# Optimization experiments

Measured on AMD Instinct MI355X. Metric: run time of the kernel, lower is better.

The kernel has to match this reference:

```python
import jax, jax.numpy as jnp
import numpy as np

B, N, D = 4, 4096, 128


def setup_inputs() -> dict:
    key = jax.random.key(0)
    k1, k2, k3 = jax.random.split(key, 3)
    x = jax.random.normal(k1, (B, N, D), dtype=jnp.float32)
    # random 0/1 adjacency (float, matching torch usage where adj>0 is masked)
    adj_mat = jax.random.randint(k2, (B, N, N), 0, 2).astype(jnp.float32)
    # xavier_normal_ for square [D, D]: std = sqrt(2 / (D + D))
    U = jax.random.normal(k3, (D, D), dtype=jnp.float32) * np.sqrt(2.0 / (D + D))
    return {"x": x, "adj_mat": adj_mat, "U": U}


def reference(x, adj_mat, U):
    # per-node loop in the original is equivalent to a masked adj^T matmul:
    # new_x[b,i,:] = relu( (sum_j 1[adj[b,j,i] > 0] * x[b,j,:]) @ U / deg[b,i] )
    # with deg = adj.sum(axis=1), i.e. deg[b,i] = sum_j adj[b,j,i].
    mask = (adj_mat > 0).astype(x.dtype)            # [B, N, N]
    deg = jnp.sum(adj_mat, axis=1)                  # [B, N]
    agg = jnp.einsum("bji,bjd->bid", mask, x)       # [B, N, D]
    out = jax.nn.relu(jnp.einsum("bid,de->bie", agg, U) / deg[..., None])
    return out
```

## Files before the change

kernel.cpp:

```cpp
#include <hip/hip_runtime.h>
#include <hip/hip_bf16.h>
#include <stdint.h>

#define BB 4
#define NN 4096
#define DD 128
#define BI 64
#define BJ 64

typedef _Float16 f16;
typedef __attribute__((ext_vector_type(8))) _Float16 f16x8;
typedef __attribute__((ext_vector_type(4))) float f32x4;

typedef __attribute__((address_space(3))) uint32_t lds_u32_t;
typedef const __attribute__((address_space(1))) uint32_t glb_u32_t;

__device__ __forceinline__ void gload_lds16(const void* g, void* l) {
    __builtin_amdgcn_global_load_lds((glb_u32_t*)g, (lds_u32_t*)l, 16, 0, 0);
}

__global__ void prep_xt(const float* __restrict__ x, f16* __restrict__ xt) {
    __shared__ float tile[32][33];
    int bid = blockIdx.x;
    int b = bid >> 9;
    int rest = bid & 511;
    int j0 = (rest >> 2) * 32;
    int d0 = (rest & 3) * 32;
    int t = threadIdx.x;
#pragma unroll
    for (int p = 0; p < 4; ++p) {
        int idx = p * 256 + t;
        int jj = idx >> 5, dd = idx & 31;
        tile[jj][dd] = x[((size_t)b * NN + j0 + jj) * DD + d0 + dd];
    }
    __syncthreads();
#pragma unroll
    for (int p = 0; p < 4; ++p) {
        int idx = p * 256 + t;
        int dd = idx >> 5, jj = idx & 31;
        xt[((size_t)b * DD + d0 + dd) * NN + j0 + jj] = (f16)tile[jj][dd];
    }
}

__global__ void prep_ut(const float* __restrict__ U, f16* __restrict__ ut) {
    __shared__ float tile[32][33];
    int bid = blockIdx.x;
    int d0 = (bid >> 2) * 32, e0 = (bid & 3) * 32;
    int t = threadIdx.x;
#pragma unroll
    for (int p = 0; p < 4; ++p) {
        int idx = p * 256 + t;
        int dd = idx >> 5, ee = idx & 31;
        tile[dd][ee] = U[(size_t)(d0 + dd) * DD + e0 + ee];
    }
    __syncthreads();
#pragma unroll
    for (int p = 0; p < 4; ++p) {
        int idx = p * 256 + t;
        int ee = idx >> 5, dd = idx & 31;
        ut[(size_t)(e0 + ee) * DD + d0 + dd] = (f16)tile[dd][ee];
    }
}

__global__ __launch_bounds__(512, 2) void agg_kernel(
    const float* __restrict__ adj, const f16* __restrict__ xt,
    float* __restrict__ agg, float* __restrict__ deg)
{
    __shared__ __align__(16) f16 mlds[2][BI * BJ];
    __shared__ __align__(16) f16 xlds[2][DD * BJ];
    __shared__ float degl[8][BI];

    const int t = threadIdx.x;
    const int w = t >> 6;
    const int l = t & 63;
    const int bid = blockIdx.x;
    const int b = bid >> 6;
    const int i0 = (bid & 63) * BI;

    const float* adjb = adj + (size_t)b * NN * NN + i0;
    const f16* xtb = xt + (size_t)b * DD * NN;

    const int si = l;
    const int su = w;
    const int mwoff = (si * 8 + (su ^ ((si >> 1) & 7))) * 8;

    const int ifr = (w & 3) * 16;
    const int dbase = (w >> 2) * 64;

    f32x4 acc[4] = {f32x4{0,0,0,0}, f32x4{0,0,0,0}, f32x4{0,0,0,0}, f32x4{0,0,0,0}};
    float degp = 0.f;

    auto stage = [&](int jt, int buf) {
        const int j0 = jt * BJ;
#pragma unroll
        for (int c = 0; c < 2; ++c) {
            int g = (w * 2 + c) * 64 + l;
            int d = g >> 3, ul = g & 7;
            int ug = ul ^ ((d >> 1) & 7);
            gload_lds16(xtb + (size_t)d * NN + j0 + ug * 8, &xlds[buf][(size_t)g * 8]);
        }
        const float* src = adjb + (size_t)(j0 + su * 8) * NN + si;
        float v[8];
#pragma unroll
        for (int q = 0; q < 8; ++q) v[q] = src[(size_t)q * NN];
        f16x8 m8;
#pragma unroll
        for (int q = 0; q < 8; ++q) {
            degp += v[q];
            m8[q] = v[q] > 0.f ? (f16)1.f : (f16)0.f;
        }
        *(f16x8*)&mlds[buf][mwoff] = m8;
    };

    auto compute = [&](int buf) {
#pragma unroll
        for (int kk = 0; kk < 2; ++kk) {
            const int row = ifr + (l & 15);
            const int ug = kk * 4 + (l >> 4);
            f16x8 a = *(const f16x8*)&mlds[buf][(row * 8 + (ug ^ ((row >> 1) & 7))) * 8];
#pragma unroll
            for (int f = 0; f < 4; ++f) {
                const int d = dbase + f * 16 + (l & 15);
                f16x8 bb = *(const f16x8*)&xlds[buf][(d * 8 + (ug ^ ((d >> 1) & 7))) * 8];
                acc[f] = __builtin_amdgcn_mfma_f32_16x16x32_f16(a, bb, acc[f], 0, 0, 0);
            }
        }
    };

    stage(0, 0);
    for (int jt = 0; jt < NN / BJ; ++jt) {
        const int cur = jt & 1;
        __syncthreads();
        if (jt + 1 < NN / BJ) stage(jt + 1, cur ^ 1);
        compute(cur);
    }

    degl[w][l] = degp;
    __syncthreads();
    if (t < BI) {
        float s = 0.f;
#pragma unroll
        for (int q = 0; q < 8; ++q) s += degl[q][t];
        deg[b * NN + i0 + t] = s;
    }

    float* aggb = agg + ((size_t)b * NN + i0) * DD;
#pragma unroll
    for (int f = 0; f < 4; ++f) {
#pragma unroll
        for (int r = 0; r < 4; ++r) {
            int row = ifr + (l >> 4) * 4 + r;
            int col = dbase + f * 16 + (l & 15);
            aggb[(size_t)row * DD + col] = acc[f][r];
        }
    }
}

__global__ __launch_bounds__(256, 2) void out_kernel(
    const float* __restrict__ agg, const f16* __restrict__ ut,
    const float* __restrict__ deg, float* __restrict__ out)
{
    __shared__ __align__(16) f16 alds[64 * DD];
    __shared__ __align__(16) f16 ulds[DD * DD];

    const int t = threadIdx.x;
    const int w = t >> 6, l = t & 63;
    const int row0 = blockIdx.x * 64;

#pragma unroll
    for (int c = 0; c < 8; ++c) {
        int g = (w * 8 + c) * 64 + l;
        int e = g >> 4, ul = g & 15;
        int ug = ul ^ (e & 7);
        gload_lds16(ut + (size_t)e * DD + ug * 8, &ulds[(size_t)g * 8]);
    }
#pragma unroll
    for (int p = 0; p < 4; ++p) {
        int chunk = p * 256 + t;
        int row = chunk >> 4, ug = chunk & 15;
        const float* src = agg + (size_t)(row0 + row) * DD + ug * 8;
        f16x8 tmp;
#pragma unroll
        for (int q = 0; q < 8; ++q) tmp[q] = (f16)src[q];
        *(f16x8*)&alds[(row * 16 + (ug ^ (row & 7))) * 8] = tmp;
    }
    __syncthreads();

    f32x4 acc[8] = {f32x4{0,0,0,0}, f32x4{0,0,0,0}, f32x4{0,0,0,0}, f32x4{0,0,0,0},
                    f32x4{0,0,0,0}, f32x4{0,0,0,0}, f32x4{0,0,0,0}, f32x4{0,0,0,0}};
#pragma unroll
    for (int kk = 0; kk < 4; ++kk) {
        const int row = w * 16 + (l & 15);
        const int ug = kk * 4 + (l >> 4);
        f16x8 a = *(const f16x8*)&alds[(row * 16 + (ug ^ (row & 7))) * 8];
#pragma unroll
        for (int ef = 0; ef < 8; ++ef) {
            const int e = ef * 16 + (l & 15);
            f16x8 bb = *(const f16x8*)&ulds[(e * 16 + (ug ^ (e & 7))) * 8];
            acc[ef] = __builtin_amdgcn_mfma_f32_16x16x32_f16(a, bb, acc[ef], 0, 0, 0);
        }
    }

    float rdeg[4];
#pragma unroll
    for (int r = 0; r < 4; ++r)
        rdeg[r] = 1.0f / deg[row0 + w * 16 + (l >> 4) * 4 + r];

    float* outb = out + (size_t)(row0 + w * 16) * DD;
#pragma unroll
    for (int ef = 0; ef < 8; ++ef) {
#pragma unroll
        for (int r = 0; r < 4; ++r) {
            float vv = acc[ef][r] * rdeg[r];
            outb[(size_t)((l >> 4) * 4 + r) * DD + ef * 16 + (l & 15)] = vv > 0.f ? vv : 0.f;
        }
    }
}

extern "C" void kernel_launch(void* const* d_in, const int* in_sizes, int n_in,
                              void* d_out, int out_size, void* d_ws, size_t ws_size,
                              hipStream_t stream) {
    const float* x   = (const float*)d_in[0];
    const float* adj = (const float*)d_in[1];
    const float* U   = (const float*)d_in[2];
    float* out = (float*)d_out;

    char* ws = (char*)d_ws;
    f16* xt  = (f16*)ws;
    f16* ut  = (f16*)(ws + (size_t)BB * DD * NN * 2);
    float* agg = (float*)(ws + (size_t)BB * DD * NN * 2 + DD * DD * 2);
    float* deg = (float*)((char*)agg + (size_t)BB * NN * DD * 4);

    hipLaunchKernelGGL(prep_xt, dim3(BB * (NN / 32) * (DD / 32)), dim3(256), 0, stream, x, xt);
    hipLaunchKernelGGL(prep_ut, dim3((DD / 32) * (DD / 32)), dim3(256), 0, stream, U, ut);
    hipLaunchKernelGGL(agg_kernel, dim3(BB * (NN / BI)), dim3(512), 0, stream, adj, xt, agg, deg);
    hipLaunchKernelGGL(out_kernel, dim3((BB * NN) / 64), dim3(256), 0, stream, agg, ut, deg, out);
}
```

Measured before the change: 384.9 us.

## Fuse output GEMM into aggregation kernel and prefetch adj into registers before compute

The per-tile adjacency loads are now issued into registers before the MFMA compute on the current buffer, and converted to the f16 mask afterwards, so global load latency overlaps with compute. The separate output kernel is fused into the aggregation kernel's epilogue: the accumulator is written to LDS as f16, U is DMA'd into reused LDS, and the degree-scaled ReLU output is written directly. This removes the fp32 agg/deg round trip through global memory and one launch. The cost is higher register pressure from holding the prefetched values, plus a longer epilogue per block.

Result: no change. 383.0 us (-0.5%).

```diff
diff --git a/kernel.cpp b/kernel.cpp
--- a/kernel.cpp
+++ b/kernel.cpp
@@ -7,6 +7,7 @@
 #define DD 128
 #define BI 64
 #define BJ 64
+#define NT (NN / BJ)
 
 typedef _Float16 f16;
 typedef __attribute__((ext_vector_type(8))) _Float16 f16x8;
@@ -62,13 +63,14 @@
     }
 }
 
-__global__ __launch_bounds__(512, 2) void agg_kernel(
+__global__ __launch_bounds__(512, 2) void fused_kernel(
     const float* __restrict__ adj, const f16* __restrict__ xt,
-    float* __restrict__ agg, float* __restrict__ deg)
+    const f16* __restrict__ ut, float* __restrict__ out)
 {
     __shared__ __align__(16) f16 mlds[2][BI * BJ];
     __shared__ __align__(16) f16 xlds[2][DD * BJ];
     __shared__ float degl[8][BI];
+    __shared__ float degs[BI];
 
     const int t = threadIdx.x;
     const int w = t >> 6;
@@ -89,8 +91,14 @@
 
     f32x4 acc[4] = {f32x4{0,0,0,0}, f32x4{0,0,0,0}, f32x4{0,0,0,0}, f32x4{0,0,0,0}};
     float degp = 0.f;
-
-    auto stage = [&](int jt, int buf) {
+    float v[8];
+
+    auto load_adj = [&](int jt) {
+        const float* src = adjb + (size_t)(jt * BJ + su * 8) * NN + si;
+#pragma unroll
+        for (int q = 0; q < 8; ++q) v[q] = src[(size_t)q * NN];
+    };
+    auto dma_xt = [&](int jt, int buf) {
         const int j0 = jt * BJ;
 #pragma unroll
         for (int c = 0; c < 2; ++c) {
@@ -99,10 +107,8 @@
             int ug = ul ^ ((d >> 1) & 7);
             gload_lds16(xtb + (size_t)d * NN + j0 + ug * 8, &xlds[buf][(size_t)g * 8]);
         }
-        const float* src = adjb + (size_t)(j0 + su * 8) * NN + si;
-        float v[8];
-#pragma unroll
-        for (int q = 0; q < 8; ++q) v[q] = src[(size_t)q * NN];
+    };
+    auto convert_write = [&](int buf) {
         f16x8 m8;
 #pragma unroll
         for (int q = 0; q < 8; ++q) {
@@ -111,7 +117,6 @@
         }
         *(f16x8*)&mlds[buf][mwoff] = m8;
     };
-
     auto compute = [&](int buf) {
 #pragma unroll
         for (int kk = 0; kk < 2; ++kk) {
@@ -127,92 +132,82 @@
         }
     };
 
-    stage(0, 0);
-    for (int jt = 0; jt < NN / BJ; ++jt) {
+    load_adj(0);
+    dma_xt(0, 0);
+    convert_write(0);
+    __syncthreads();
+
+    for (int jt = 0; jt < NT; ++jt) {
         const int cur = jt & 1;
+        if (jt + 1 < NT) {
+            load_adj(jt + 1);
+            dma_xt(jt + 1, cur ^ 1);
+        }
+        compute(cur);
+        if (jt + 1 < NT) convert_write(cur ^ 1);
         __syncthreads();
-        if (jt + 1 < NN / BJ) stage(jt + 1, cur ^ 1);
-        compute(cur);
     }
 
     degl[w][l] = degp;
     __syncthreads();
-    if (t < BI) {
-        float s = 0.f;
-#pragma unroll
-        for (int q = 0; q < 8; ++q) s += degl[q][t];
-        deg[b * NN + i0 + t] = s;
-    }
-
-    float* aggb = agg + ((size_t)b * NN + i0) * DD;
+
+    f16* alds = &mlds[0][0];
+    f16* ulds = &xlds[0][0];
+
+#pragma unroll
+    for (int c = 0; c < 4; ++c) {
+        int g = (w * 4 + c) * 64 + l;
+        int e = g >> 4, ul = g & 15;
+        int ug = ul ^ (e & 7);
+        gload_lds16(ut + (size_t)e * DD + ug * 8, &ulds[(size_t)g * 8]);
+    }
 #pragma unroll
     for (int f = 0; f < 4; ++f) {
 #pragma unroll
         for (int r = 0; r < 4; ++r) {
             int row = ifr + (l >> 4) * 4 + r;
             int col = dbase + f * 16 + (l & 15);
-            aggb[(size_t)row * DD + col] = acc[f][r];
-        }
-    }
-}
-
-__global__ __launch_bounds__(256, 2) void out_kernel(
-    const float* __restrict__ agg, const f16* __restrict__ ut,
-    const float* __restrict__ deg, float* __restrict__ out)
-{
-    __shared__ __align__(16) f16 alds[64 * DD];
-    __shared__ __align__(16) f16 ulds[DD * DD];
-
-    const int t = threadIdx.x;
-    const int w = t >> 6, l = t & 63;
-    const int row0 = blockIdx.x * 64;
-
-#pragma unroll
-    for (int c = 0; c < 8; ++c) {
-        int g = (w * 8 + c) * 64 + l;
-        int e = g >> 4, ul = g & 15;
-        int ug = ul ^ (e & 7);
-        gload_lds16(ut + (size_t)e * DD + ug * 8, &ulds[(size_t)g * 8]);
-    }
-#pragma unroll
-    for (int p = 0; p < 4; ++p) {
-        int chunk = p * 256 + t;
-        int row = chunk >> 4, ug = chunk & 15;
-        const float* src = agg + (size_t)(row0 + row) * DD + ug * 8;
-        f16x8 tmp;
-#pragma unroll
-        for (int q = 0; q < 8; ++q) tmp[q] = (f16)src[q];
-        *(f16x8*)&alds[(row * 16 + (ug ^ (row & 7))) * 8] = tmp;
-    }
-    __syncthreads();
-
-    f32x4 acc[8] = {f32x4{0,0,0,0}, f32x4{0,0,0,0}, f32x4{0,0,0,0}, f32x4{0,0,0,0},
-                    f32x4{0,0,0,0}, f32x4{0,0,0,0}, f32x4{0,0,0,0}, f32x4{0,0,0,0}};
+            alds[(row * 16 + ((col >> 3) ^ (row & 7))) * 8 + (col & 7)] = (f16)acc[f][r];
+        }
+    }
+    if (t < BI) {
+        float s = 0.f;
+#pragma unroll
+        for (int q = 0; q < 8; ++q) s += degl[q][t];
+        degs[t] = s;
+    }
+    __syncthreads();
+
+    const int ifr2 = (w & 3) * 16;
+    const int ebase = (w >> 2) * 64;
+    f32x4 acc2[4] = {f32x4{0,0,0,0}, f32x4{0,0,0,0}, f32x4{0,0,0,0}, f32x4{0,0,0,0}};
 #pragma unroll
     for (int kk = 0; kk < 4; ++kk) {
-        const int row = w * 16 + (l & 15);
+        const int row = ifr2 + (l & 15);
         const int ug = kk * 4 + (l >> 4);
         f16x8 a = *(const f16x8*)&alds[(row * 16 + (ug ^ (row & 7))) * 8];
 #pragma unroll
-        for (int ef = 0; ef < 8; ++ef) {
-            const int e = ef * 16 + (l & 15);
+        for (int ef = 0; ef < 4; ++ef) {
+            const int e = ebase + ef * 16 + (l & 15);
             f16x8 bb = *(const f16x8*)&ulds[(e * 16 + (ug ^ (e & 7))) * 8];
-            acc[ef] = __builtin_amdgcn_mfma_f32_16x16x32_f16(a, bb, acc[ef], 0, 0, 0);
+            acc2[ef] = __builtin_amdgcn_mfma_f32_16x16x32_f16(a, bb, acc2[ef], 0, 0, 0);
         }
     }
 
     float rdeg[4];
 #pragma unroll
     for (int r = 0; r < 4; ++r)
-        rdeg[r] = 1.0f / deg[row0 + w * 16 + (l >> 4) * 4 + r];
-
-    float* outb = out + (size_t)(row0 + w * 16) * DD;
-#pragma unroll
-    for (int ef = 0; ef < 8; ++ef) {
+        rdeg[r] = 1.0f / degs[ifr2 + (l >> 4) * 4 + r];
+
+    float* outb = out + ((size_t)b * NN + i0) * DD;
+#pragma unroll
+    for (int ef = 0; ef < 4; ++ef) {
 #pragma unroll
         for (int r = 0; r < 4; ++r) {
-            float vv = acc[ef][r] * rdeg[r];
-            outb[(size_t)((l >> 4) * 4 + r) * DD + ef * 16 + (l & 15)] = vv > 0.f ? vv : 0.f;
+            int row = ifr2 + (l >> 4) * 4 + r;
+            int e = ebase + ef * 16 + (l & 15);
+            float vv = acc2[ef][r] * rdeg[r];
+            outb[(size_t)row * DD + e] = vv > 0.f ? vv : 0.f;
         }
     }
 }
@@ -226,13 +221,10 @@
     float* out = (float*)d_out;
 
     char* ws = (char*)d_ws;
-    f16* xt  = (f16*)ws;
-    f16* ut  = (f16*)(ws + (size_t)BB * DD * NN * 2);
-    float* agg = (float*)(ws + (size_t)BB * DD * NN * 2 + DD * DD * 2);
-    float* deg = (float*)((char*)agg + (size_t)BB * NN * DD * 4);
+    f16* xt = (f16*)ws;
+    f16* ut = (f16*)(ws + (size_t)BB * DD * NN * 2);
 
     hipLaunchKernelGGL(prep_xt, dim3(BB * (NN / 32) * (DD / 32)), dim3(256), 0, stream, x, xt);
     hipLaunchKernelGGL(prep_ut, dim3((DD / 32) * (DD / 32)), dim3(256), 0, stream, U, ut);
-    hipLaunchKernelGGL(agg_kernel, dim3(BB * (NN / BI)), dim3(512), 0, stream, adj, xt, agg, deg);
-    hipLaunchKernelGGL(out_kernel, dim3((BB * NN) / 64), dim3(256), 0, stream, agg, ut, deg, out);
-}
+    hipLaunchKernelGGL(fused_kernel, dim3(BB * (NN / BI)), dim3(512), 0, stream, adj, xt, ut, out);
+}
```
